# Kernel tuning notes

Measured on AMD Instinct MI355X. Metric: run time of the kernel, lower is better.

## Reference

```python
import jax, jax.numpy as jnp
import numpy as np

M, N, K = 4096, 8192, 4096


def setup_inputs() -> dict:
    key = jax.random.key(0)
    k1, k2, k3, k4 = jax.random.split(key, 4)
    a = jax.random.randint(k1, (M, K), 0, 127, dtype=jnp.int32)  # int8 activations
    b = jax.random.randint(k2, (N, K), 0, 127, dtype=jnp.int32)  # int8 weights (row-major [N,K])
    alpha_row = jax.random.uniform(k3, (M, 1), dtype=jnp.float16)  # per-row dequant scale
    alpha_col = jax.random.uniform(k4, (1, N), dtype=jnp.float16)  # per-col dequant scale
    return {"a": a, "b": b, "alpha_row": alpha_row, "alpha_col": alpha_col}


def reference(a, b, alpha_row, alpha_col):
    # x = a @ b.T in fp32 (int8 values upcast), then rescale by outer product of scales
    x = jnp.matmul(a.astype(jnp.float32), b.astype(jnp.float32).T)  # [M, N]
    scale = alpha_row.astype(jnp.float32) * alpha_col.astype(jnp.float32)  # [M, N] via broadcast
    out = x * scale
    return out.astype(jnp.float16)
```

## Files before the change

### kernel.cpp

```cpp
#include <hip/hip_runtime.h>
#include <cstdint>
#include <cstddef>

#define M_DIM 4096
#define N_DIM 8192
#define K_DIM 4096

typedef __attribute__((ext_vector_type(4))) int int4v;

__global__ void __launch_bounds__(256) pack_frag(const int* __restrict__ a,
                                                 const int* __restrict__ b,
                                                 unsigned char* __restrict__ pa,
                                                 unsigned char* __restrict__ pb) {
    size_t t = (size_t)blockIdx.x * 256 + threadIdx.x;
    const size_t NA = (size_t)(M_DIM / 16) * (K_DIM / 64) * 64;
    const int* __restrict__ src;
    unsigned char* __restrict__ dst;
    if (t < NA) {
        src = a; dst = pa;
    } else {
        src = b; dst = pb; t -= NA;
    }
    const int l = (int)(t & 63);
    const int s = (int)((t >> 6) & 63);
    const int p = (int)(t >> 12);
    const int* g = src + ((size_t)(16 * p + (l & 15))) * K_DIM + s * 64 + (l >> 4) * 16;
    const int4v* g4 = (const int4v*)g;
    int4v o;
#pragma unroll
    for (int q = 0; q < 4; ++q) {
        int4v v = g4[q];
        o[q] = (v[0] & 0xff) | ((v[1] & 0xff) << 8) | ((v[2] & 0xff) << 16) | (v[3] << 24);
    }
    ((int4v*)dst)[t] = o;
}

__device__ inline void async_copy16(const unsigned char* g, unsigned char* l) {
    __builtin_amdgcn_global_load_lds(
        (const __attribute__((address_space(1))) void*)g,
        (__attribute__((address_space(3))) void*)l,
        16, 0, 0);
}

#define BAR() __builtin_amdgcn_s_barrier()

__global__ void __launch_bounds__(256, 2) gemm_i8(const unsigned char* __restrict__ Ap,
                                                  const unsigned char* __restrict__ Bp,
                                                  const _Float16* __restrict__ arow,
                                                  const _Float16* __restrict__ acol,
                                                  _Float16* __restrict__ Cout) {
    __shared__ __align__(16) unsigned char lds[3 * 24576];

    const int tid  = threadIdx.x;
    const int lane = tid & 63;
    const int wave = tid >> 6;
    const int bn   = blockIdx.x;
    const int bm   = blockIdx.y;

    const int pm0 = (wave & 1) * 4;
    const int pn0 = (wave >> 1) * 8;

    const unsigned char* ag[2];
    int salo[2];
#pragma unroll
    for (int r = 0; r < 2; ++r) {
        const int p = 2 * wave + r;
        ag[r]   = Ap + (size_t)(bm * 8 + p) * 65536 + lane * 16;
        salo[r] = p * 1024;
    }
    const unsigned char* bg[4];
    int sblo[4];
#pragma unroll
    for (int r = 0; r < 4; ++r) {
        const int p = 4 * wave + r;
        bg[r]   = Bp + (size_t)(bn * 16 + p) * 65536 + lane * 16;
        sblo[r] = 8192 + p * 1024;
    }

    const int a_off = pm0 * 1024 + lane * 16;
    const int b_off = 8192 + pn0 * 1024 + lane * 16;

    int4v acc[4][8];
#pragma unroll
    for (int i = 0; i < 4; ++i)
#pragma unroll
        for (int j = 0; j < 8; ++j) acc[i][j] = (int4v)0;

    const int NT = K_DIM / 64;

#pragma unroll
    for (int t = 0; t < 2; ++t) {
        const size_t gk = (size_t)t * 1024;
        const int lo = t * 24576;
#pragma unroll
        for (int r = 0; r < 2; ++r) async_copy16(ag[r] + gk, lds + lo + salo[r]);
#pragma unroll
        for (int r = 0; r < 4; ++r) async_copy16(bg[r] + gk, lds + lo + sblo[r]);
    }
    asm volatile("s_waitcnt vmcnt(6)" ::: "memory");
    BAR();

    int o_cur = 0, o_nxt = 24576, o_pre = 49152;

#pragma unroll 3
    for (int T = 0; T < NT; ++T) {
        const bool pre = (T + 2 < NT);
        const unsigned char* Ac = lds + o_cur;

        if (pre) {
            const size_t gk2 = (size_t)(T + 2) * 1024;
#pragma unroll
            for (int r = 0; r < 2; ++r)
                async_copy16(ag[r] + gk2, lds + o_pre + salo[r]);
#pragma unroll
            for (int r = 0; r < 4; ++r)
                async_copy16(bg[r] + gk2, lds + o_pre + sblo[r]);
        }

        int4v af[4], bf[8];
#pragma unroll
        for (int i = 0; i < 4; ++i)
            af[i] = *(const int4v*)(Ac + a_off + i * 1024);
#pragma unroll
        for (int j = 0; j < 8; ++j)
            bf[j] = *(const int4v*)(Ac + b_off + j * 1024);

        __builtin_amdgcn_s_setprio(1);
#pragma unroll
        for (int i = 0; i < 4; ++i)
#pragma unroll
            for (int j = 0; j < 8; ++j)
                acc[i][j] = __builtin_amdgcn_mfma_i32_16x16x64_i8(af[i], bf[j],
                                                                  acc[i][j], 0, 0, 0);
        __builtin_amdgcn_s_setprio(0);

        if (pre) {
            asm volatile("s_waitcnt vmcnt(6)" ::: "memory");
        } else {
            asm volatile("s_waitcnt vmcnt(0)" ::: "memory");
        }
        BAR();

        const int t0 = o_cur; o_cur = o_nxt; o_nxt = o_pre; o_pre = t0;
    }

    const int gcol0 = bn * 256 + pn0 * 16 + (lane & 15);
    float ac8[8];
#pragma unroll
    for (int j = 0; j < 8; ++j) ac8[j] = (float)acol[gcol0 + j * 16];

    const size_t grow0 = (size_t)bm * 128 + pm0 * 16 + (lane >> 4) * 4;
#pragma unroll
    for (int i = 0; i < 4; ++i) {
#pragma unroll
        for (int r = 0; r < 4; ++r) {
            const size_t row = grow0 + i * 16 + r;
            const float ar = (float)arow[row];
            _Float16* outp = Cout + row * (size_t)N_DIM + gcol0;
#pragma unroll
            for (int j = 0; j < 8; ++j) {
                float v = (float)acc[i][j][r] * ar * ac8[j];
                outp[j * 16] = (_Float16)v;
            }
        }
    }
}

extern "C" void kernel_launch(void* const* d_in, const int* in_sizes, int n_in,
                              void* d_out, int out_size, void* d_ws, size_t ws_size,
                              hipStream_t stream) {
    const int* a = (const int*)d_in[0];
    const int* b = (const int*)d_in[1];
    const _Float16* ar = (const _Float16*)d_in[2];
    const _Float16* ac = (const _Float16*)d_in[3];
    _Float16* out = (_Float16*)d_out;

    unsigned char* pa = (unsigned char*)d_ws;
    unsigned char* pb = pa + (size_t)M_DIM * K_DIM;

    const size_t total_frag = (size_t)(M_DIM / 16 + N_DIM / 16) * (K_DIM / 64) * 64;
    pack_frag<<<(int)(total_frag / 256), 256, 0, stream>>>(a, b, pa, pb);

    dim3 grid(N_DIM / 256, M_DIM / 128);
    gemm_i8<<<grid, 256, 0, stream>>>(pa, pb, ar, ac, out);
}
```

Measured before the change: 359.2 us.

## Deepen LDS pipeline to four stages and double-buffer register fragments

The int8 GEMM main loop now uses four LDS stages, prefetching three tiles ahead instead of two. It also ping-pongs two sets of A/B fragment registers, loading the next tile from LDS while the MFMAs run on the current one. The loop is manually unrolled by two to alternate the register sets. The aim is to hide LDS and global-load latency inside each wave. In exchange, LDS grows to 96KB and the launch bound drops to one block per CU, which halves occupancy and raises register pressure.

Measured after the change: 405.3 us. 1.13x slower.

```diff
diff --git a/kernel.cpp b/kernel.cpp
--- a/kernel.cpp
+++ b/kernel.cpp
@@ -44,12 +44,12 @@
 
 #define BAR() __builtin_amdgcn_s_barrier()
 
-__global__ void __launch_bounds__(256, 2) gemm_i8(const unsigned char* __restrict__ Ap,
+__global__ void __launch_bounds__(256, 1) gemm_i8(const unsigned char* __restrict__ Ap,
                                                   const unsigned char* __restrict__ Bp,
                                                   const _Float16* __restrict__ arow,
                                                   const _Float16* __restrict__ acol,
                                                   _Float16* __restrict__ Cout) {
-    __shared__ __align__(16) unsigned char lds[3 * 24576];
+    __shared__ __align__(16) unsigned char lds[4 * 24576];
 
     const int tid  = threadIdx.x;
     const int lane = tid & 63;
@@ -89,7 +89,7 @@
     const int NT = K_DIM / 64;
 
 #pragma unroll
-    for (int t = 0; t < 2; ++t) {
+    for (int t = 0; t < 3; ++t) {
         const size_t gk = (size_t)t * 1024;
         const int lo = t * 24576;
 #pragma unroll
@@ -100,48 +100,78 @@
     asm volatile("s_waitcnt vmcnt(6)" ::: "memory");
     BAR();
 
-    int o_cur = 0, o_nxt = 24576, o_pre = 49152;
-
-#pragma unroll 3
-    for (int T = 0; T < NT; ++T) {
-        const bool pre = (T + 2 < NT);
-        const unsigned char* Ac = lds + o_cur;
-
-        if (pre) {
-            const size_t gk2 = (size_t)(T + 2) * 1024;
-#pragma unroll
-            for (int r = 0; r < 2; ++r)
-                async_copy16(ag[r] + gk2, lds + o_pre + salo[r]);
-#pragma unroll
-            for (int r = 0; r < 4; ++r)
-                async_copy16(bg[r] + gk2, lds + o_pre + sblo[r]);
+    int4v af0[4], bf0[8], af1[4], bf1[8];
+#pragma unroll
+    for (int i = 0; i < 4; ++i) af0[i] = *(const int4v*)(lds + a_off + i * 1024);
+#pragma unroll
+    for (int j = 0; j < 8; ++j) bf0[j] = *(const int4v*)(lds + b_off + j * 1024);
+
+#pragma unroll 1
+    for (int u = 0; u < NT / 2; ++u) {
+        {
+            const int T = 2 * u;
+            if (T + 3 < NT) {
+                const size_t gk = (size_t)(T + 3) * 1024;
+                const int lo = ((T + 3) & 3) * 24576;
+#pragma unroll
+                for (int r = 0; r < 2; ++r) async_copy16(ag[r] + gk, lds + lo + salo[r]);
+#pragma unroll
+                for (int r = 0; r < 4; ++r) async_copy16(bg[r] + gk, lds + lo + sblo[r]);
+            }
+            {
+                const unsigned char* Rb = lds + ((T + 1) & 3) * 24576;
+#pragma unroll
+                for (int i = 0; i < 4; ++i) af1[i] = *(const int4v*)(Rb + a_off + i * 1024);
+#pragma unroll
+                for (int j = 0; j < 8; ++j) bf1[j] = *(const int4v*)(Rb + b_off + j * 1024);
+            }
+            __builtin_amdgcn_s_setprio(1);
+#pragma unroll
+            for (int i = 0; i < 4; ++i)
+#pragma unroll
+                for (int j = 0; j < 8; ++j)
+                    acc[i][j] = __builtin_amdgcn_mfma_i32_16x16x64_i8(af0[i], bf0[j],
+                                                                      acc[i][j], 0, 0, 0);
+            __builtin_amdgcn_s_setprio(0);
+            if (T + 3 < NT) {
+                asm volatile("s_waitcnt vmcnt(6)" ::: "memory");
+            } else {
+                asm volatile("s_waitcnt vmcnt(0)" ::: "memory");
+            }
+            BAR();
         }
-
-        int4v af[4], bf[8];
-#pragma unroll
-        for (int i = 0; i < 4; ++i)
-            af[i] = *(const int4v*)(Ac + a_off + i * 1024);
-#pragma unroll
-        for (int j = 0; j < 8; ++j)
-            bf[j] = *(const int4v*)(Ac + b_off + j * 1024);
-
-        __builtin_amdgcn_s_setprio(1);
-#pragma unroll
-        for (int i = 0; i < 4; ++i)
-#pragma unroll
-            for (int j = 0; j < 8; ++j)
-                acc[i][j] = __builtin_amdgcn_mfma_i32_16x16x64_i8(af[i], bf[j],
-                                                                  acc[i][j], 0, 0, 0);
-        __builtin_amdgcn_s_setprio(0);
-
-        if (pre) {
-            asm volatile("s_waitcnt vmcnt(6)" ::: "memory");
-        } else {
-            asm volatile("s_waitcnt vmcnt(0)" ::: "memory");
+        {
+            const int T = 2 * u + 1;
+            if (T + 3 < NT) {
+                const size_t gk = (size_t)(T + 3) * 1024;
+                const int lo = ((T + 3) & 3) * 24576;
+#pragma unroll
+                for (int r = 0; r < 2; ++r) async_copy16(ag[r] + gk, lds + lo + salo[r]);
+#pragma unroll
+                for (int r = 0; r < 4; ++r) async_copy16(bg[r] + gk, lds + lo + sblo[r]);
+            }
+            if (T + 1 < NT) {
+                const unsigned char* Rb = lds + ((T + 1) & 3) * 24576;
+#pragma unroll
+                for (int i = 0; i < 4; ++i) af0[i] = *(const int4v*)(Rb + a_off + i * 1024);
+#pragma unroll
+                for (int j = 0; j < 8; ++j) bf0[j] = *(const int4v*)(Rb + b_off + j * 1024);
+            }
+            __builtin_amdgcn_s_setprio(1);
+#pragma unroll
+            for (int i = 0; i < 4; ++i)
+#pragma unroll
+                for (int j = 0; j < 8; ++j)
+                    acc[i][j] = __builtin_amdgcn_mfma_i32_16x16x64_i8(af1[i], bf1[j],
+                                                                      acc[i][j], 0, 0, 0);
+            __builtin_amdgcn_s_setprio(0);
+            if (T + 3 < NT) {
+                asm volatile("s_waitcnt vmcnt(6)" ::: "memory");
+            } else {
+                asm volatile("s_waitcnt vmcnt(0)" ::: "memory");
+            }
+            BAR();
         }
-        BAR();
-
-        const int t0 = o_cur; o_cur = o_nxt; o_nxt = o_pre; o_pre = t0;
     }
 
     const int gcol0 = bn * 256 + pn0 * 16 + (lane & 15);
```
